# Kernel tuning notes

Measured on AMD Instinct MI355X. Metric: run time of the kernel, lower is better.

The kernel has to match this reference:

```python
import jax, jax.numpy as jnp
import numpy as np

# pywt db8 reconstruction low-pass filter (rec_lo); other filters derived per pywt conventions
_REC_LO = np.array([
    0.05441584224308161, 0.3128715909144659, 0.6756307362980128,
    0.5853546836548691, -0.015829105256023893, -0.2840155429624281,
    0.00047248457399797254, 0.128747426620186, -0.01736930100202211,
    -0.04408825393106472, 0.013981027917015516, 0.008746094047015655,
    -0.00487035299301066, -0.0003917403729959771, 0.0006754494059985568,
    -0.00011747678400228192], dtype=np.float64)
_F = 16
_REC_HI = np.array([(-1.0) ** k * _REC_LO[_F - 1 - k] for k in range(_F)])  # qmf
_DEC_LO = _REC_LO[::-1].copy()
_DEC_HI = _REC_HI[::-1].copy()
# lax.conv does cross-correlation; np.convolve flips the filter, so pre-flip here
_DEC_K = np.ascontiguousarray(np.stack([_DEC_LO[::-1], _DEC_HI[::-1]])[:, None, :])  # [2,1,F]
_REC_K = np.ascontiguousarray(np.stack([_REC_LO[::-1], _REC_HI[::-1]])[None, :, :])  # [1,2,F]
_THRESHOLD_FACTOR = 1.0


def _dwt_last(x):
    # single-level DWT along last axis, pywt 'symmetric' boundary mode
    shp = x.shape
    xf = x.reshape(-1, 1, shp[-1])
    xe = jnp.pad(xf, ((0, 0), (0, 0), (_F - 1, _F - 1)), mode='symmetric')[:, :, 1:]
    y = jax.lax.conv_general_dilated(xe, jnp.asarray(_DEC_K, x.dtype), (2,), 'VALID',
                                     dimension_numbers=('NCW', 'OIW', 'NCW'))  # [M,2,n]
    n = y.shape[-1]  # n = floor((N + F - 1) / 2)
    return y[:, 0].reshape(shp[:-1] + (n,)), y[:, 1].reshape(shp[:-1] + (n,))


def _idwt_last(ca, cd, out_len):
    # single-level inverse DWT along last axis; out_len = 2*n - F + 2
    shp = ca.shape
    n = shp[-1]
    m = int(np.prod(shp[:-1]))
    u = jnp.zeros((m, 2, 2 * n), ca.dtype)
    u = u.at[:, 0, ::2].set(ca.reshape(m, n)).at[:, 1, ::2].set(cd.reshape(m, n))
    ue = jnp.pad(u, ((0, 0), (0, 0), (_F - 1, _F - 1)))
    y = jax.lax.conv_general_dilated(ue, jnp.asarray(_REC_K, ca.dtype), (1,), 'VALID',
                                     dimension_numbers=('NCW', 'OIW', 'NCW'))[:, 0]
    return y[:, _F - 2:_F - 2 + out_len].reshape(shp[:-1] + (out_len,))


def _forward(x):
    B, H, W, C = x.shape
    M = B * C
    xm = jnp.transpose(x, (0, 3, 1, 2)).reshape(M, H, W)
    # level-1 wavedec2: rows (W axis) then columns (H axis)
    lo, hi = _dwt_last(xm)                               # [M,H,nW]
    ll, lh = _dwt_last(jnp.swapaxes(lo, -1, -2))         # [M,nW,nH]
    hl, hh = _dwt_last(jnp.swapaxes(hi, -1, -2))         # [M,nW,nH]
    # universal threshold from median abs of all detail subbands, per sample/channel
    det = jnp.concatenate([lh.reshape(M, -1), hl.reshape(M, -1), hh.reshape(M, -1)], axis=-1)
    sigma = jnp.median(jnp.abs(det), axis=-1) / 0.6745
    t = (sigma * jnp.sqrt(2.0 * jnp.log(float(H * W))) * _THRESHOLD_FACTOR)[:, None, None]
    soft = lambda c: jnp.sign(c) * jnp.maximum(jnp.abs(c) - t, 0.0)
    lh, hl, hh = soft(lh), soft(hl), soft(hh)
    # waverec2: inverse along H then along W
    nH = ll.shape[-1]
    Hr = 2 * nH - _F + 2
    rl = jnp.swapaxes(_idwt_last(ll, lh, Hr), -1, -2)    # [M,Hr,nW]
    rh = jnp.swapaxes(_idwt_last(hl, hh, Hr), -1, -2)    # [M,Hr,nW]
    nW = rl.shape[-1]
    y = _idwt_last(rl, rh, 2 * nW - _F + 2)              # [M,Hr,Wr]
    y = y[:, :H, :W].reshape(B, C, H, W)
    return jnp.transpose(y, (0, 2, 3, 1)).astype(x.dtype)


def setup_inputs() -> dict:
    key = jax.random.key(0)
    x = jax.random.normal(key, (32, 512, 512, 3), dtype=jnp.float32)
    return {"x": x}


def reference(x):
    return _forward(x)
```

## Files before the change

kernel.cpp:

```cpp
#include <hip/hip_runtime.h>
#include <math.h>

#define B_   32
#define H_   512
#define W_   512
#define C_   3
#define M_   96
#define NW_  263
#define NH_  263
#define DETPER 69169
#define DETTOT 207507
#define KRANK  103753u

__device__ __constant__ float RLO[16] = {
    0.05441584224308161f,  0.3128715909144659f,   0.6756307362980128f,
    0.5853546836548691f,  -0.015829105256023893f, -0.2840155429624281f,
    0.00047248457399797254f, 0.128747426620186f,  -0.01736930100202211f,
   -0.04408825393106472f,  0.013981027917015516f,  0.008746094047015655f,
   -0.00487035299301066f, -0.0003917403729959771f, 0.0006754494059985568f,
   -0.00011747678400228192f};
__device__ __constant__ float RHI[16] = {
   -0.00011747678400228192f, -0.0006754494059985568f, -0.0003917403729959771f,
    0.00487035299301066f,     0.008746094047015655f,  -0.013981027917015516f,
   -0.04408825393106472f,     0.01736930100202211f,    0.128747426620186f,
   -0.00047248457399797254f, -0.2840155429624281f,     0.015829105256023893f,
    0.5853546836548691f,     -0.6756307362980128f,     0.3128715909144659f,
   -0.05441584224308161f};

__device__ __forceinline__ int symmap(int p, int N) {
    int q = p - 14;
    if (q < 0)  return -q - 1;
    if (q >= N) return 2 * N - 1 - q;
    return q;
}

__device__ __forceinline__ float softthr(float v, float thr) {
    float a = fabsf(v) - thr;
    return a > 0.f ? copysignf(a, v) : 0.f;
}

__device__ __forceinline__ unsigned detbits(const float* lh, const float* hl,
                                            const float* hh, int m, int i) {
    const float* p; int ii;
    if (i < DETPER)          { p = lh; ii = i; }
    else if (i < 2 * DETPER) { p = hl; ii = i - DETPER; }
    else                     { p = hh; ii = i - 2 * DETPER; }
    return __float_as_uint(fabsf(p[(size_t)m * DETPER + ii]));
}

__global__ __launch_bounds__(256) void k_rowdwt(const float* __restrict__ x,
                                                float* __restrict__ lo,
                                                float* __restrict__ hi) {
    __shared__ float row[W_ * C_];
    const int hrow = blockIdx.x, b = blockIdx.y, tid = threadIdx.x;
    const float* src = x + (size_t)(b * H_ + hrow) * (W_ * C_);
    for (int i = tid; i < W_ * C_; i += 256) row[i] = src[i];
    __syncthreads();
    for (int task = tid; task < C_ * NW_; task += 256) {
        int j = task % NW_, c = task / NW_;
        float al = 0.f, ah = 0.f;
#pragma unroll
        for (int k = 0; k < 16; ++k) {
            int w = symmap(2 * j + k, W_);
            float v = row[w * C_ + c];
            al = fmaf(v, RLO[k], al);
            ah = fmaf(v, RHI[k], ah);
        }
        size_t o = ((size_t)((b * C_ + c) * H_ + hrow)) * NW_ + j;
        lo[o] = al;
        hi[o] = ah;
    }
}

__global__ __launch_bounds__(256) void k_coldwt(const float* __restrict__ lo,
                                                const float* __restrict__ hi,
                                                float* __restrict__ ll, float* __restrict__ lh,
                                                float* __restrict__ hl, float* __restrict__ hh) {
    const int tx = threadIdx.x & 63, ty = threadIdx.x >> 6;
    const int jw = blockIdx.x * 64 + tx;
    const int jh = blockIdx.y * 4 + ty;
    const int m = blockIdx.z;
    if (jw >= NW_ || jh >= NH_) return;
    const float* pl = lo + (size_t)m * H_ * NW_;
    const float* ph = hi + (size_t)m * H_ * NW_;
    float a0 = 0.f, a1 = 0.f, a2 = 0.f, a3 = 0.f;
#pragma unroll
    for (int k = 0; k < 16; ++k) {
        int h = symmap(2 * jh + k, H_);
        float vl = pl[(size_t)h * NW_ + jw];
        float vh = ph[(size_t)h * NW_ + jw];
        a0 = fmaf(vl, RLO[k], a0);
        a1 = fmaf(vl, RHI[k], a1);
        a2 = fmaf(vh, RLO[k], a2);
        a3 = fmaf(vh, RHI[k], a3);
    }
    size_t o = ((size_t)m * NH_ + jh) * NW_ + jw;
    ll[o] = a0; lh[o] = a1; hl[o] = a2; hh[o] = a3;
}

__global__ __launch_bounds__(256) void k_hist1(const float* __restrict__ lh,
                                               const float* __restrict__ hl,
                                               const float* __restrict__ hh,
                                               unsigned* __restrict__ hist) {
    __shared__ unsigned h[2048];
    const int tid = threadIdx.x, m = blockIdx.x;
    for (int i = tid; i < 2048; i += 256) h[i] = 0u;
    __syncthreads();
    const int stride = gridDim.y * 256;
    for (int i = blockIdx.y * 256 + tid; i < DETTOT; i += stride) {
        unsigned u = detbits(lh, hl, hh, m, i);
        atomicAdd(&h[u >> 21], 1u);
    }
    __syncthreads();
    for (int i = tid; i < 2048; i += 256)
        if (h[i]) atomicAdd(&hist[m * 2048 + i], h[i]);
}

__global__ __launch_bounds__(256) void k_hist2(const float* __restrict__ lh,
                                               const float* __restrict__ hl,
                                               const float* __restrict__ hh,
                                               const int* __restrict__ selBin1,
                                               unsigned* __restrict__ hist) {
    __shared__ unsigned h[2048];
    const int tid = threadIdx.x, m = blockIdx.x;
    const unsigned target = (unsigned)selBin1[m];
    for (int i = tid; i < 2048; i += 256) h[i] = 0u;
    __syncthreads();
    const int stride = gridDim.y * 256;
    for (int i = blockIdx.y * 256 + tid; i < DETTOT; i += stride) {
        unsigned u = detbits(lh, hl, hh, m, i);
        if ((u >> 21) == target) atomicAdd(&h[(u >> 10) & 0x7FFu], 1u);
    }
    __syncthreads();
    for (int i = tid; i < 2048; i += 256)
        if (h[i]) atomicAdd(&hist[m * 2048 + i], h[i]);
}

__global__ __launch_bounds__(256) void k_hist3(const float* __restrict__ lh,
                                               const float* __restrict__ hl,
                                               const float* __restrict__ hh,
                                               const int* __restrict__ selBin1,
                                               const int* __restrict__ selBin2,
                                               unsigned* __restrict__ hist) {
    __shared__ unsigned h[1024];
    const int tid = threadIdx.x, m = blockIdx.x;
    const unsigned target = ((unsigned)selBin1[m] << 11) | (unsigned)selBin2[m];
    for (int i = tid; i < 1024; i += 256) h[i] = 0u;
    __syncthreads();
    const int stride = gridDim.y * 256;
    for (int i = blockIdx.y * 256 + tid; i < DETTOT; i += stride) {
        unsigned u = detbits(lh, hl, hh, m, i);
        if ((u >> 10) == target) atomicAdd(&h[u & 0x3FFu], 1u);
    }
    __syncthreads();
    for (int i = tid; i < 1024; i += 256)
        if (h[i]) atomicAdd(&hist[m * 1024 + i], h[i]);
}

__device__ int histSelect(unsigned* hist, int nb, unsigned rank, unsigned* rem) {
    __shared__ unsigned ps[256];
    __shared__ int s_bin;
    __shared__ unsigned s_rem;
    const int tid = threadIdx.x;
    const int per = nb >> 8;
    unsigned s = 0;
    for (int i = 0; i < per; ++i) s += hist[tid * per + i];
    ps[tid] = s;
    __syncthreads();
    for (int off = 1; off < 256; off <<= 1) {
        unsigned v = ps[tid];
        unsigned add = (tid >= off) ? ps[tid - off] : 0u;
        __syncthreads();
        ps[tid] = v + add;
        __syncthreads();
    }
    unsigned incl = ps[tid], excl = incl - s;
    if (rank >= excl && rank < incl) {
        unsigned cum = excl;
        for (int i = 0; i < per; ++i) {
            unsigned c = hist[tid * per + i];
            if (cum + c > rank) { s_bin = tid * per + i; s_rem = rank - cum; break; }
            cum += c;
        }
    }
    __syncthreads();
    int rbin = s_bin;
    unsigned rr = s_rem;
    __syncthreads();
    *rem = rr;
    return rbin;
}

__global__ __launch_bounds__(256) void k_sel2048(const unsigned* __restrict__ hist,
                                                 const unsigned* __restrict__ rankIn,
                                                 int* __restrict__ selBin,
                                                 unsigned* __restrict__ rankOut) {
    __shared__ unsigned h[2048];
    const int m = blockIdx.x, tid = threadIdx.x;
    for (int i = tid; i < 2048; i += 256) h[i] = hist[m * 2048 + i];
    __syncthreads();
    unsigned rank = rankIn ? rankIn[m] : KRANK;
    unsigned rem;
    int bin = histSelect(h, 2048, rank, &rem);
    if (tid == 0) { selBin[m] = bin; rankOut[m] = rem; }
}

__global__ __launch_bounds__(256) void k_sel3(const unsigned* __restrict__ hist,
                                              const unsigned* __restrict__ rankIn,
                                              const int* __restrict__ selBin1,
                                              const int* __restrict__ selBin2,
                                              float* __restrict__ tval) {
    __shared__ unsigned h[1024];
    const int m = blockIdx.x, tid = threadIdx.x;
    for (int i = tid; i < 1024; i += 256) h[i] = hist[m * 1024 + i];
    __syncthreads();
    unsigned rem;
    int low = histSelect(h, 1024, rankIn[m], &rem);
    if (tid == 0) {
        unsigned bits = ((unsigned)selBin1[m] << 21) | ((unsigned)selBin2[m] << 10) | (unsigned)low;
        double med = (double)__uint_as_float(bits);
        tval[m] = (float)(med / 0.6745 * 4.995327667046959);
    }
}

__global__ __launch_bounds__(256) void k_colidwt(const float* __restrict__ ll,
                                                 const float* __restrict__ lh,
                                                 const float* __restrict__ hl,
                                                 const float* __restrict__ hh,
                                                 const float* __restrict__ tval,
                                                 float* __restrict__ rl,
                                                 float* __restrict__ rh) {
    const int tx = threadIdx.x & 63, ty = threadIdx.x >> 6;
    const int jw = blockIdx.x * 64 + tx;
    const int t = blockIdx.y * 4 + ty;
    const int m = blockIdx.z;
    if (jw >= NW_) return;
    const float thr = tval[m];
    const int s = t >> 1, r = t & 1;
    float aL = 0.f, aH = 0.f;
    const size_t mb = (size_t)m * NH_ * NW_;
#pragma unroll
    for (int a = 0; a < 8; ++a) {
        int jh = s + 7 - a;
        size_t o = mb + (size_t)jh * NW_ + jw;
        float wl = RLO[2 * a + r], wh = RHI[2 * a + r];
        float vll = ll[o];
        float vlh = softthr(lh[o], thr);
        float vhl = softthr(hl[o], thr);
        float vhh = softthr(hh[o], thr);
        aL = fmaf(vll, wl, fmaf(vlh, wh, aL));
        aH = fmaf(vhl, wl, fmaf(vhh, wh, aH));
    }
    size_t o = ((size_t)m * H_ + t) * NW_ + jw;
    rl[o] = aL;
    rh[o] = aH;
}

__global__ __launch_bounds__(256) void k_rowidwt(const float* __restrict__ rl,
                                                 const float* __restrict__ rh,
                                                 float* __restrict__ out) {
    __shared__ float rlr[C_ * NW_], rhr[C_ * NW_];
    const int hrow = blockIdx.x, b = blockIdx.y, tid = threadIdx.x;
    for (int i = tid; i < C_ * NW_; i += 256) {
        int c = i / NW_, j = i - c * NW_;
        size_t o = ((size_t)((b * C_ + c) * H_) + hrow) * NW_ + j;
        rlr[i] = rl[o];
        rhr[i] = rh[o];
    }
    __syncthreads();
    float* dst = out + (size_t)(b * H_ + hrow) * (W_ * C_);
    for (int task = tid; task < W_ * C_; task += 256) {
        int w = task / C_, c = task - C_ * (task / C_);
        int s = w >> 1, r = w & 1;
        float acc = 0.f;
#pragma unroll
        for (int a = 0; a < 8; ++a) {
            int j = s + 7 - a;
            acc = fmaf(rlr[c * NW_ + j], RLO[2 * a + r],
                       fmaf(rhr[c * NW_ + j], RHI[2 * a + r], acc));
        }
        dst[task] = acc;
    }
}

extern "C" void kernel_launch(void* const* d_in, const int* in_sizes, int n_in,
                              void* d_out, int out_size, void* d_ws, size_t ws_size,
                              hipStream_t stream) {
    const float* x = (const float*)d_in[0];
    float* out = (float*)d_out;

    char* ws = (char*)d_ws;
    const size_t LOSZ = (size_t)M_ * H_ * NW_;
    const size_t SBSZ = (size_t)M_ * NH_ * NW_;
    float* lo = (float*)ws; ws += LOSZ * 4;
    float* hi = (float*)ws; ws += LOSZ * 4;
    float* ll = (float*)ws; ws += SBSZ * 4;
    float* lh = (float*)ws; ws += SBSZ * 4;
    float* hl = (float*)ws; ws += SBSZ * 4;
    float* hh = (float*)ws; ws += SBSZ * 4;
    unsigned* hist1 = (unsigned*)ws; ws += (size_t)M_ * 2048 * 4;
    unsigned* hist2 = (unsigned*)ws; ws += (size_t)M_ * 2048 * 4;
    unsigned* hist3 = (unsigned*)ws; ws += (size_t)M_ * 1024 * 4;
    int*      selBin1 = (int*)ws;      ws += M_ * 4;
    int*      selBin2 = (int*)ws;      ws += M_ * 4;
    unsigned* rank1   = (unsigned*)ws; ws += M_ * 4;
    unsigned* rank2   = (unsigned*)ws; ws += M_ * 4;
    float*    tval    = (float*)ws;    ws += M_ * 4;
    float* rl = lo;
    float* rh = hi;

    hipMemsetAsync(hist1, 0, (size_t)M_ * (2048 + 2048 + 1024) * 4, stream);

    k_rowdwt <<<dim3(H_, B_),     256, 0, stream>>>(x, lo, hi);
    k_coldwt <<<dim3(5, 66, M_),  256, 0, stream>>>(lo, hi, ll, lh, hl, hh);
    k_hist1  <<<dim3(M_, 16),     256, 0, stream>>>(lh, hl, hh, hist1);
    k_sel2048<<<dim3(M_),         256, 0, stream>>>(hist1, nullptr, selBin1, rank1);
    k_hist2  <<<dim3(M_, 16),     256, 0, stream>>>(lh, hl, hh, selBin1, hist2);
    k_sel2048<<<dim3(M_),         256, 0, stream>>>(hist2, rank1, selBin2, rank2);
    k_hist3  <<<dim3(M_, 16),     256, 0, stream>>>(lh, hl, hh, selBin1, selBin2, hist3);
    k_sel3   <<<dim3(M_),         256, 0, stream>>>(hist3, rank2, selBin1, selBin2, tval);
    k_colidwt<<<dim3(5, 128, M_), 256, 0, stream>>>(ll, lh, hl, hh, tval, rl, rh);
    k_rowidwt<<<dim3(H_, B_),     256, 0, stream>>>(rl, rh, out);
}
```

Baseline: 514.4 us.

## Fuse row/column DWT and IDWT into tiled shared-memory kernels, vectorize histograms

Merges the row and column forward DWT into one tiled kernel that keeps intermediate lo/hi rows in shared memory, and likewise fuses column and row inverse DWT with soft thresholding into a single tiled kernel writing the output directly. This removes the global round-trips through the lo/hi and rl/rh buffers. Detail subbands are stored contiguously per sample so the histogram passes can use float4 loads without a per-element branch. The cost is halo recomputation at tile edges, larger shared memory per block, and strided channel-interleaved global loads and stores.

```diff
diff --git a/kernel.cpp b/kernel.cpp
--- a/kernel.cpp
+++ b/kernel.cpp
@@ -10,6 +10,8 @@
 #define NH_  263
 #define DETPER 69169
 #define DETTOT 207507
+#define DETSTRIDE 207508
+#define NVEC 51876
 #define KRANK  103753u
 
 __device__ __constant__ float RLO[16] = {
@@ -27,8 +29,7 @@
     0.5853546836548691f,     -0.6756307362980128f,     0.3128715909144659f,
    -0.05441584224308161f};
 
-__device__ __forceinline__ int symmap(int p, int N) {
-    int q = p - 14;
+__device__ __forceinline__ int refl(int q, int N) {
     if (q < 0)  return -q - 1;
     if (q >= N) return 2 * N - 1 - q;
     return q;
@@ -39,76 +40,89 @@
     return a > 0.f ? copysignf(a, v) : 0.f;
 }
 
-__device__ __forceinline__ unsigned detbits(const float* lh, const float* hl,
-                                            const float* hh, int m, int i) {
-    const float* p; int ii;
-    if (i < DETPER)          { p = lh; ii = i; }
-    else if (i < 2 * DETPER) { p = hl; ii = i - DETPER; }
-    else                     { p = hh; ii = i - 2 * DETPER; }
-    return __float_as_uint(fabsf(p[(size_t)m * DETPER + ii]));
-}
-
-__global__ __launch_bounds__(256) void k_rowdwt(const float* __restrict__ x,
-                                                float* __restrict__ lo,
-                                                float* __restrict__ hi) {
-    __shared__ float row[W_ * C_];
-    const int hrow = blockIdx.x, b = blockIdx.y, tid = threadIdx.x;
-    const float* src = x + (size_t)(b * H_ + hrow) * (W_ * C_);
-    for (int i = tid; i < W_ * C_; i += 256) row[i] = src[i];
-    __syncthreads();
-    for (int task = tid; task < C_ * NW_; task += 256) {
-        int j = task % NW_, c = task / NW_;
+__global__ __launch_bounds__(256) void k_zero(unsigned* __restrict__ p, int n) {
+    int i = blockIdx.x * 256 + threadIdx.x;
+    if (i < n) p[i] = 0u;
+}
+
+__global__ __launch_bounds__(256) void k_fwd(const float* __restrict__ x,
+                                             float* __restrict__ ll,
+                                             float* __restrict__ det) {
+    __shared__ float sX[46 * 144];
+    __shared__ float sLO[46 * 64], sHI[46 * 64];
+    const int m   = blockIdx.x;
+    const int jw0 = blockIdx.y * 64;
+    const int jh0 = blockIdx.z * 16;
+    const int b = m / 3, c = m - 3 * (m / 3);
+    const int tid = threadIdx.x;
+    const int prow0 = 2 * jh0 - 14, pcol0 = 2 * jw0 - 14;
+    for (int l = tid; l < 46 * 142; l += 256) {
+        int rr = l / 142, cl = l - rr * 142;
+        int h = refl(prow0 + rr, H_);
+        int w = refl(pcol0 + cl, W_);
+        sX[rr * 144 + cl] = x[((size_t)(b * H_ + h) * W_ + w) * C_ + c];
+    }
+    __syncthreads();
+    for (int l = tid; l < 46 * 64; l += 256) {
+        int rr = l >> 6, j = l & 63;
+        const float* px = &sX[rr * 144 + 2 * j];
         float al = 0.f, ah = 0.f;
 #pragma unroll
         for (int k = 0; k < 16; ++k) {
-            int w = symmap(2 * j + k, W_);
-            float v = row[w * C_ + c];
-            al = fmaf(v, RLO[k], al);
-            ah = fmaf(v, RHI[k], ah);
-        }
-        size_t o = ((size_t)((b * C_ + c) * H_ + hrow)) * NW_ + j;
-        lo[o] = al;
-        hi[o] = ah;
-    }
-}
-
-__global__ __launch_bounds__(256) void k_coldwt(const float* __restrict__ lo,
-                                                const float* __restrict__ hi,
-                                                float* __restrict__ ll, float* __restrict__ lh,
-                                                float* __restrict__ hl, float* __restrict__ hh) {
-    const int tx = threadIdx.x & 63, ty = threadIdx.x >> 6;
-    const int jw = blockIdx.x * 64 + tx;
-    const int jh = blockIdx.y * 4 + ty;
-    const int m = blockIdx.z;
-    if (jw >= NW_ || jh >= NH_) return;
-    const float* pl = lo + (size_t)m * H_ * NW_;
-    const float* ph = hi + (size_t)m * H_ * NW_;
-    float a0 = 0.f, a1 = 0.f, a2 = 0.f, a3 = 0.f;
-#pragma unroll
-    for (int k = 0; k < 16; ++k) {
-        int h = symmap(2 * jh + k, H_);
-        float vl = pl[(size_t)h * NW_ + jw];
-        float vh = ph[(size_t)h * NW_ + jw];
-        a0 = fmaf(vl, RLO[k], a0);
-        a1 = fmaf(vl, RHI[k], a1);
-        a2 = fmaf(vh, RLO[k], a2);
-        a3 = fmaf(vh, RHI[k], a3);
-    }
-    size_t o = ((size_t)m * NH_ + jh) * NW_ + jw;
-    ll[o] = a0; lh[o] = a1; hl[o] = a2; hh[o] = a3;
-}
-
-__global__ __launch_bounds__(256) void k_hist1(const float* __restrict__ lh,
-                                               const float* __restrict__ hl,
-                                               const float* __restrict__ hh,
+            al = fmaf(px[k], RLO[k], al);
+            ah = fmaf(px[k], RHI[k], ah);
+        }
+        sLO[l] = al;
+        sHI[l] = ah;
+    }
+    __syncthreads();
+    const int tx = tid & 63, ty = tid >> 6;
+    const int jw = jw0 + tx;
+    if (jw >= NW_) return;
+    float* llp = ll + (size_t)m * DETPER;
+    float* dp  = det + (size_t)m * DETSTRIDE;
+#pragma unroll
+    for (int i = 0; i < 4; ++i) {
+        int dy = ty + 4 * i;
+        int jh = jh0 + dy;
+        if (jh >= NH_) continue;
+        int rbase = 2 * dy;
+        float a0 = 0.f, a1 = 0.f, a2 = 0.f, a3 = 0.f;
+#pragma unroll
+        for (int k = 0; k < 16; ++k) {
+            float vl = sLO[(rbase + k) * 64 + tx];
+            float vh = sHI[(rbase + k) * 64 + tx];
+            a0 = fmaf(vl, RLO[k], a0);
+            a1 = fmaf(vl, RHI[k], a1);
+            a2 = fmaf(vh, RLO[k], a2);
+            a3 = fmaf(vh, RHI[k], a3);
+        }
+        size_t o = (size_t)jh * NW_ + jw;
+        llp[o] = a0;
+        dp[o] = a1;
+        dp[DETPER + o] = a2;
+        dp[2 * DETPER + o] = a3;
+    }
+}
+
+__global__ __launch_bounds__(256) void k_hist1(const float* __restrict__ det,
                                                unsigned* __restrict__ hist) {
     __shared__ unsigned h[2048];
     const int tid = threadIdx.x, m = blockIdx.x;
     for (int i = tid; i < 2048; i += 256) h[i] = 0u;
     __syncthreads();
+    const float* dp = det + (size_t)m * DETSTRIDE;
+    const float4* dp4 = (const float4*)dp;
     const int stride = gridDim.y * 256;
-    for (int i = blockIdx.y * 256 + tid; i < DETTOT; i += stride) {
-        unsigned u = detbits(lh, hl, hh, m, i);
+    for (int v = blockIdx.y * 256 + tid; v < NVEC; v += stride) {
+        float4 f = dp4[v];
+        atomicAdd(&h[__float_as_uint(fabsf(f.x)) >> 21], 1u);
+        atomicAdd(&h[__float_as_uint(fabsf(f.y)) >> 21], 1u);
+        atomicAdd(&h[__float_as_uint(fabsf(f.z)) >> 21], 1u);
+        atomicAdd(&h[__float_as_uint(fabsf(f.w)) >> 21], 1u);
+    }
+    if (blockIdx.y == 0 && tid < DETTOT - 4 * NVEC) {
+        unsigned u = __float_as_uint(fabsf(dp[4 * NVEC + tid]));
         atomicAdd(&h[u >> 21], 1u);
     }
     __syncthreads();
@@ -116,9 +130,7 @@
         if (h[i]) atomicAdd(&hist[m * 2048 + i], h[i]);
 }
 
-__global__ __launch_bounds__(256) void k_hist2(const float* __restrict__ lh,
-                                               const float* __restrict__ hl,
-                                               const float* __restrict__ hh,
+__global__ __launch_bounds__(256) void k_hist2(const float* __restrict__ det,
                                                const int* __restrict__ selBin1,
                                                unsigned* __restrict__ hist) {
     __shared__ unsigned h[2048];
@@ -126,9 +138,22 @@
     const unsigned target = (unsigned)selBin1[m];
     for (int i = tid; i < 2048; i += 256) h[i] = 0u;
     __syncthreads();
+    const float* dp = det + (size_t)m * DETSTRIDE;
+    const float4* dp4 = (const float4*)dp;
     const int stride = gridDim.y * 256;
-    for (int i = blockIdx.y * 256 + tid; i < DETTOT; i += stride) {
-        unsigned u = detbits(lh, hl, hh, m, i);
+    for (int v = blockIdx.y * 256 + tid; v < NVEC; v += stride) {
+        float4 f = dp4[v];
+        unsigned a = __float_as_uint(fabsf(f.x));
+        unsigned b = __float_as_uint(fabsf(f.y));
+        unsigned c = __float_as_uint(fabsf(f.z));
+        unsigned d = __float_as_uint(fabsf(f.w));
+        if ((a >> 21) == target) atomicAdd(&h[(a >> 10) & 0x7FFu], 1u);
+        if ((b >> 21) == target) atomicAdd(&h[(b >> 10) & 0x7FFu], 1u);
+        if ((c >> 21) == target) atomicAdd(&h[(c >> 10) & 0x7FFu], 1u);
+        if ((d >> 21) == target) atomicAdd(&h[(d >> 10) & 0x7FFu], 1u);
+    }
+    if (blockIdx.y == 0 && tid < DETTOT - 4 * NVEC) {
+        unsigned u = __float_as_uint(fabsf(dp[4 * NVEC + tid]));
         if ((u >> 21) == target) atomicAdd(&h[(u >> 10) & 0x7FFu], 1u);
     }
     __syncthreads();
@@ -136,9 +161,7 @@
         if (h[i]) atomicAdd(&hist[m * 2048 + i], h[i]);
 }
 
-__global__ __launch_bounds__(256) void k_hist3(const float* __restrict__ lh,
-                                               const float* __restrict__ hl,
-                                               const float* __restrict__ hh,
+__global__ __launch_bounds__(256) void k_hist3(const float* __restrict__ det,
                                                const int* __restrict__ selBin1,
                                                const int* __restrict__ selBin2,
                                                unsigned* __restrict__ hist) {
@@ -147,9 +170,22 @@
     const unsigned target = ((unsigned)selBin1[m] << 11) | (unsigned)selBin2[m];
     for (int i = tid; i < 1024; i += 256) h[i] = 0u;
     __syncthreads();
+    const float* dp = det + (size_t)m * DETSTRIDE;
+    const float4* dp4 = (const float4*)dp;
     const int stride = gridDim.y * 256;
-    for (int i = blockIdx.y * 256 + tid; i < DETTOT; i += stride) {
-        unsigned u = detbits(lh, hl, hh, m, i);
+    for (int v = blockIdx.y * 256 + tid; v < NVEC; v += stride) {
+        float4 f = dp4[v];
+        unsigned a = __float_as_uint(fabsf(f.x));
+        unsigned b = __float_as_uint(fabsf(f.y));
+        unsigned c = __float_as_uint(fabsf(f.z));
+        unsigned d = __float_as_uint(fabsf(f.w));
+        if ((a >> 10) == target) atomicAdd(&h[a & 0x3FFu], 1u);
+        if ((b >> 10) == target) atomicAdd(&h[b & 0x3FFu], 1u);
+        if ((c >> 10) == target) atomicAdd(&h[c & 0x3FFu], 1u);
+        if ((d >> 10) == target) atomicAdd(&h[d & 0x3FFu], 1u);
+    }
+    if (blockIdx.y == 0 && tid < DETTOT - 4 * NVEC) {
+        unsigned u = __float_as_uint(fabsf(dp[4 * NVEC + tid]));
         if ((u >> 10) == target) atomicAdd(&h[u & 0x3FFu], 1u);
     }
     __syncthreads();
@@ -162,6 +198,7 @@
     __shared__ int s_bin;
     __shared__ unsigned s_rem;
     const int tid = threadIdx.x;
+    if (tid == 0) { s_bin = 0; s_rem = 0; }
     const int per = nb >> 8;
     unsigned s = 0;
     for (int i = 0; i < per; ++i) s += hist[tid * per + i];
@@ -223,63 +260,56 @@
     }
 }
 
-__global__ __launch_bounds__(256) void k_colidwt(const float* __restrict__ ll,
-                                                 const float* __restrict__ lh,
-                                                 const float* __restrict__ hl,
-                                                 const float* __restrict__ hh,
-                                                 const float* __restrict__ tval,
-                                                 float* __restrict__ rl,
-                                                 float* __restrict__ rh) {
-    const int tx = threadIdx.x & 63, ty = threadIdx.x >> 6;
-    const int jw = blockIdx.x * 64 + tx;
-    const int t = blockIdx.y * 4 + ty;
-    const int m = blockIdx.z;
-    if (jw >= NW_) return;
+__global__ __launch_bounds__(256) void k_inv(const float* __restrict__ ll,
+                                             const float* __restrict__ det,
+                                             const float* __restrict__ tval,
+                                             float* __restrict__ out) {
+    __shared__ float sLL[23 * 40], sLH[23 * 40], sHL[23 * 40], sHH[23 * 40];
+    __shared__ float sRL[32 * 40], sRH[32 * 40];
+    const int m  = blockIdx.x;
+    const int w0 = blockIdx.y * 64;
+    const int t0 = blockIdx.z * 32;
+    const int b = m / 3, c = m - 3 * (m / 3);
+    const int tid = threadIdx.x;
     const float thr = tval[m];
-    const int s = t >> 1, r = t & 1;
-    float aL = 0.f, aH = 0.f;
-    const size_t mb = (size_t)m * NH_ * NW_;
-#pragma unroll
-    for (int a = 0; a < 8; ++a) {
-        int jh = s + 7 - a;
-        size_t o = mb + (size_t)jh * NW_ + jw;
-        float wl = RLO[2 * a + r], wh = RHI[2 * a + r];
-        float vll = ll[o];
-        float vlh = softthr(lh[o], thr);
-        float vhl = softthr(hl[o], thr);
-        float vhh = softthr(hh[o], thr);
-        aL = fmaf(vll, wl, fmaf(vlh, wh, aL));
-        aH = fmaf(vhl, wl, fmaf(vhh, wh, aH));
-    }
-    size_t o = ((size_t)m * H_ + t) * NW_ + jw;
-    rl[o] = aL;
-    rh[o] = aH;
-}
-
-__global__ __launch_bounds__(256) void k_rowidwt(const float* __restrict__ rl,
-                                                 const float* __restrict__ rh,
-                                                 float* __restrict__ out) {
-    __shared__ float rlr[C_ * NW_], rhr[C_ * NW_];
-    const int hrow = blockIdx.x, b = blockIdx.y, tid = threadIdx.x;
-    for (int i = tid; i < C_ * NW_; i += 256) {
-        int c = i / NW_, j = i - c * NW_;
-        size_t o = ((size_t)((b * C_ + c) * H_) + hrow) * NW_ + j;
-        rlr[i] = rl[o];
-        rhr[i] = rh[o];
-    }
-    __syncthreads();
-    float* dst = out + (size_t)(b * H_ + hrow) * (W_ * C_);
-    for (int task = tid; task < W_ * C_; task += 256) {
-        int w = task / C_, c = task - C_ * (task / C_);
-        int s = w >> 1, r = w & 1;
+    const int jW0 = w0 >> 1, s0 = t0 >> 1;
+    const float* llp = ll + (size_t)m * DETPER;
+    const float* dp  = det + (size_t)m * DETSTRIDE;
+    for (int l = tid; l < 23 * 39; l += 256) {
+        int rr = l / 39, cc = l - rr * 39;
+        size_t o = (size_t)(s0 + rr) * NW_ + (jW0 + cc);
+        int li = rr * 40 + cc;
+        sLL[li] = llp[o];
+        sLH[li] = softthr(dp[o], thr);
+        sHL[li] = softthr(dp[DETPER + o], thr);
+        sHH[li] = softthr(dp[2 * DETPER + o], thr);
+    }
+    __syncthreads();
+    for (int l = tid; l < 32 * 39; l += 256) {
+        int tr = l / 39, cc = l - tr * 39;
+        int srow = tr >> 1, r = tr & 1;
+        float aL = 0.f, aH = 0.f;
+#pragma unroll
+        for (int a = 0; a < 8; ++a) {
+            int li = (srow + 7 - a) * 40 + cc;
+            float wl = RLO[2 * a + r], wh = RHI[2 * a + r];
+            aL = fmaf(sLL[li], wl, fmaf(sLH[li], wh, aL));
+            aH = fmaf(sHL[li], wl, fmaf(sHH[li], wh, aH));
+        }
+        sRL[tr * 40 + cc] = aL;
+        sRH[tr * 40 + cc] = aH;
+    }
+    __syncthreads();
+    for (int l = tid; l < 32 * 64; l += 256) {
+        int tr = l >> 6, wloc = l & 63;
+        int r = wloc & 1, jb = (wloc >> 1) + 7;
         float acc = 0.f;
 #pragma unroll
         for (int a = 0; a < 8; ++a) {
-            int j = s + 7 - a;
-            acc = fmaf(rlr[c * NW_ + j], RLO[2 * a + r],
-                       fmaf(rhr[c * NW_ + j], RHI[2 * a + r], acc));
-        }
-        dst[task] = acc;
+            int li = tr * 40 + jb - a;
+            acc = fmaf(sRL[li], RLO[2 * a + r], fmaf(sRH[li], RHI[2 * a + r], acc));
+        }
+        out[((size_t)(b * H_ + (t0 + tr)) * W_ + (w0 + wloc)) * C_ + c] = acc;
     }
 }
 
@@ -290,14 +320,8 @@
     float* out = (float*)d_out;
 
     char* ws = (char*)d_ws;
-    const size_t LOSZ = (size_t)M_ * H_ * NW_;
-    const size_t SBSZ = (size_t)M_ * NH_ * NW_;
-    float* lo = (float*)ws; ws += LOSZ * 4;
-    float* hi = (float*)ws; ws += LOSZ * 4;
-    float* ll = (float*)ws; ws += SBSZ * 4;
-    float* lh = (float*)ws; ws += SBSZ * 4;
-    float* hl = (float*)ws; ws += SBSZ * 4;
-    float* hh = (float*)ws; ws += SBSZ * 4;
+    float* ll  = (float*)ws; ws += (size_t)M_ * DETPER * 4;
+    float* det = (float*)ws; ws += (size_t)M_ * DETSTRIDE * 4;
     unsigned* hist1 = (unsigned*)ws; ws += (size_t)M_ * 2048 * 4;
     unsigned* hist2 = (unsigned*)ws; ws += (size_t)M_ * 2048 * 4;
     unsigned* hist3 = (unsigned*)ws; ws += (size_t)M_ * 1024 * 4;
@@ -306,19 +330,15 @@
     unsigned* rank1   = (unsigned*)ws; ws += M_ * 4;
     unsigned* rank2   = (unsigned*)ws; ws += M_ * 4;
     float*    tval    = (float*)ws;    ws += M_ * 4;
-    float* rl = lo;
-    float* rh = hi;
-
-    hipMemsetAsync(hist1, 0, (size_t)M_ * (2048 + 2048 + 1024) * 4, stream);
-
-    k_rowdwt <<<dim3(H_, B_),     256, 0, stream>>>(x, lo, hi);
-    k_coldwt <<<dim3(5, 66, M_),  256, 0, stream>>>(lo, hi, ll, lh, hl, hh);
-    k_hist1  <<<dim3(M_, 16),     256, 0, stream>>>(lh, hl, hh, hist1);
+
+    const int histWords = M_ * (2048 + 2048 + 1024);
+    k_zero   <<<dim3((histWords + 255) / 256), 256, 0, stream>>>(hist1, histWords);
+    k_fwd    <<<dim3(M_, 5, 17),  256, 0, stream>>>(x, ll, det);
+    k_hist1  <<<dim3(M_, 16),     256, 0, stream>>>(det, hist1);
     k_sel2048<<<dim3(M_),         256, 0, stream>>>(hist1, nullptr, selBin1, rank1);
-    k_hist2  <<<dim3(M_, 16),     256, 0, stream>>>(lh, hl, hh, selBin1, hist2);
+    k_hist2  <<<dim3(M_, 16),     256, 0, stream>>>(det, selBin1, hist2);
     k_sel2048<<<dim3(M_),         256, 0, stream>>>(hist2, rank1, selBin2, rank2);
-    k_hist3  <<<dim3(M_, 16),     256, 0, stream>>>(lh, hl, hh, selBin1, selBin2, hist3);
+    k_hist3  <<<dim3(M_, 16),     256, 0, stream>>>(det, selBin1, selBin2, hist3);
     k_sel3   <<<dim3(M_),         256, 0, stream>>>(hist3, rank2, selBin1, selBin2, tval);
-    k_colidwt<<<dim3(5, 128, M_), 256, 0, stream>>>(ll, lh, hl, hh, tval, rl, rh);
-    k_rowidwt<<<dim3(H_, B_),     256, 0, stream>>>(rl, rh, out);
-}
+    k_inv    <<<dim3(M_, 8, 16),  256, 0, stream>>>(ll, det, tval, out);
+}
```

Measured after the change: 433.1 us. -15.8%, faster.
